# Optimization experiments

Measured on AMD Instinct MI355X. Metric: run time of the kernel, lower is better.

## Reference

```python
import jax, jax.numpy as jnp
import numpy as np

N = 100_000        # number of independent Markov chains (particles)
N_FRAMES = 500     # chain length (module default)
# index 0 -> identity (stay), index 1 -> swap (flip state)
T_MAT = jnp.array([[[1., 0.], [0., 1.]],
                   [[0., 1.], [1., 0.]]], dtype=jnp.float32)


def setup_inputs() -> dict:
    key = jax.random.key(0)
    idx = jax.random.randint(key, (N,), 0, 2)
    initial = jax.nn.one_hot(idx, 2, dtype=jnp.float32)  # one-hot states [N,2]
    return {"initial": initial, "seed": 0}


def reference(initial, seed):
    key = jax.random.key(seed)
    kp, ks = jax.random.split(key)
    # torch code resets transition probs once at i==0 with p = rand()*0.001
    p = jax.random.uniform(kp, (), dtype=jnp.float32) * 0.001
    # row 0: [0.8, 0.2]; row 1: [1-p, p]
    p1 = jnp.stack([jnp.float32(0.2), p])  # P(class==1) per categorical row
    keys = jax.random.split(ks, N_FRAMES)

    def step(state, k):
        # Categorical sample per (particle, row): A[n, j] ~ Bernoulli(p1[j])
        u = jax.random.uniform(k, state.shape, dtype=state.dtype)
        A = (u < p1[None, :]).astype(state.dtype)          # [N,2] in {0,1}
        t = jnp.sum(state * A, axis=-1).astype(jnp.int32)  # [N] select action
        m = T_MAT[t]                                       # [N,2,2] permutation
        new_state = jnp.einsum('nc,ncd->nd', state, m)     # [N,2]
        return new_state, new_state

    _, chain = jax.lax.scan(step, initial, keys)
    return chain  # [N_FRAMES, N, 2]
```

## Files before the change

### kernel.cpp

```cpp
#include <hip/hip_runtime.h>
#include <stdint.h>

#define N_PART   100000
#define N_FRAMES 500

__device__ __forceinline__ uint32_t rotl32(uint32_t v, int d) {
    return (v << d) | (v >> (32 - d));
}

#define TF_ROUND(r) { x0 += x1; x1 = rotl32(x1, (r)); x1 ^= x0; }

__device__ __forceinline__ void tf2x32(uint32_t k0, uint32_t k1,
                                       uint32_t x0, uint32_t x1,
                                       uint32_t &o0, uint32_t &o1) {
    const uint32_t k2 = k0 ^ k1 ^ 0x1BD11BDAu;
    x0 += k0; x1 += k1;
    TF_ROUND(13) TF_ROUND(15) TF_ROUND(26) TF_ROUND(6)
    x0 += k1; x1 += k2 + 1u;
    TF_ROUND(17) TF_ROUND(29) TF_ROUND(16) TF_ROUND(24)
    x0 += k2; x1 += k0 + 2u;
    TF_ROUND(13) TF_ROUND(15) TF_ROUND(26) TF_ROUND(6)
    x0 += k0; x1 += k1 + 3u;
    TF_ROUND(17) TF_ROUND(29) TF_ROUND(16) TF_ROUND(24)
    x0 += k1; x1 += k2 + 4u;
    TF_ROUND(13) TF_ROUND(15) TF_ROUND(26) TF_ROUND(6)
    x0 += k2; x1 += k0 + 5u;
    o0 = x0; o1 = x1;
}

__device__ __forceinline__ float uniform_from_bits(uint32_t bits) {
    return __uint_as_float((bits >> 9) | 0x3f800000u) - 1.0f;
}

__global__ __launch_bounds__(256)
void hmm_kernel(const float* __restrict__ initial,
                const int* __restrict__ seed_ptr,
                float* __restrict__ out) {
    __shared__ uint32_t skey0[N_FRAMES];
    __shared__ uint32_t skey1[N_FRAMES];
    __shared__ float sp;

    const int tid = threadIdx.x;
    const uint32_t seed_lo = (uint32_t)seed_ptr[0];
    const uint32_t seed_hi = 0u;

    uint32_t ks0, ks1;
    tf2x32(seed_hi, seed_lo, 0u, 1u, ks0, ks1);

    for (int t = tid; t < N_FRAMES; t += blockDim.x) {
        uint32_t a, b;
        tf2x32(ks0, ks1, 0u, (uint32_t)t, a, b);
        skey0[t] = a;
        skey1[t] = b;
    }
    if (tid == 0) {
        uint32_t kp0, kp1;
        tf2x32(seed_hi, seed_lo, 0u, 0u, kp0, kp1);
        uint32_t b0, b1;
        tf2x32(kp0, kp1, 0u, 0u, b0, b1);
        sp = uniform_from_bits(b0 ^ b1) * 0.001f;
    }
    __syncthreads();

    const int n = blockIdx.x * blockDim.x + tid;
    if (n >= N_PART) return;

    const float p = sp;
    const float p0 = 0.2f;

    int s = (initial[2 * n + 1] > 0.5f) ? 1 : 0;

    float2* __restrict__ outv = (float2*)out;

    for (int t = 0; t < N_FRAMES; ++t) {
        const uint32_t k0 = skey0[t];
        const uint32_t k1 = skey1[t];
        uint32_t b0, b1;
        tf2x32(k0, k1, 0u, (uint32_t)(2 * n + s), b0, b1);
        const float u = uniform_from_bits(b0 ^ b1);
        const float thr = s ? p : p0;
        s ^= (u < thr) ? 1 : 0;
        const float2 o = s ? make_float2(0.0f, 1.0f) : make_float2(1.0f, 0.0f);
        outv[(size_t)t * N_PART + n] = o;
    }
}

extern "C" void kernel_launch(void* const* d_in, const int* in_sizes, int n_in,
                              void* d_out, int out_size, void* d_ws, size_t ws_size,
                              hipStream_t stream) {
    const float* initial = (const float*)d_in[0];
    const int*   seed    = (const int*)d_in[1];
    float*       out     = (float*)d_out;

    const int block = 256;
    const int grid = (N_PART + block - 1) / block;
    hmm_kernel<<<grid, block, 0, stream>>>(initial, seed, out);
}
```

Before: 497.2 us.

## Split chain simulation into bitmap pass and vectorized streaming output kernel

```diff
diff --git a/kernel.cpp b/kernel.cpp
--- a/kernel.cpp
+++ b/kernel.cpp
@@ -3,6 +3,10 @@
 
 #define N_PART   100000
 #define N_FRAMES 500
+#define NTW      16
+#define PPB      391
+
+typedef float f32x4 __attribute__((ext_vector_type(4)));
 
 __device__ __forceinline__ uint32_t rotl32(uint32_t v, int d) {
     return (v << d) | (v >> (32 - d));
@@ -32,56 +36,75 @@
     return __uint_as_float((bits >> 9) | 0x3f800000u) - 1.0f;
 }
 
-__global__ __launch_bounds__(256)
-void hmm_kernel(const float* __restrict__ initial,
-                const int* __restrict__ seed_ptr,
-                float* __restrict__ out) {
-    __shared__ uint32_t skey0[N_FRAMES];
-    __shared__ uint32_t skey1[N_FRAMES];
-    __shared__ float sp;
+__global__ __launch_bounds__(512)
+void chain_kernel(const float* __restrict__ initial,
+                  const int* __restrict__ seed_ptr,
+                  uint32_t* __restrict__ bmp) {
+    __shared__ uint32_t sk0[N_FRAMES + 1], sk1[N_FRAMES + 1];
+    __shared__ float sp_;
 
     const int tid = threadIdx.x;
     const uint32_t seed_lo = (uint32_t)seed_ptr[0];
-    const uint32_t seed_hi = 0u;
 
-    uint32_t ks0, ks1;
-    tf2x32(seed_hi, seed_lo, 0u, 1u, ks0, ks1);
-
-    for (int t = tid; t < N_FRAMES; t += blockDim.x) {
-        uint32_t a, b;
-        tf2x32(ks0, ks1, 0u, (uint32_t)t, a, b);
-        skey0[t] = a;
-        skey1[t] = b;
+    if (tid <= N_FRAMES) {
+        uint32_t ks0, ks1, a, b;
+        tf2x32(0u, seed_lo, 0u, 1u, ks0, ks1);
+        tf2x32(ks0, ks1, 0u, (uint32_t)tid, a, b);
+        sk0[tid] = a; sk1[tid] = b;
     }
-    if (tid == 0) {
-        uint32_t kp0, kp1;
-        tf2x32(seed_hi, seed_lo, 0u, 0u, kp0, kp1);
-        uint32_t b0, b1;
+    if (tid == 511) {
+        uint32_t kp0, kp1, b0, b1;
+        tf2x32(0u, seed_lo, 0u, 0u, kp0, kp1);
         tf2x32(kp0, kp1, 0u, 0u, b0, b1);
-        sp = uniform_from_bits(b0 ^ b1) * 0.001f;
+        sp_ = uniform_from_bits(b0 ^ b1) * 0.001f;
     }
     __syncthreads();
 
-    const int n = blockIdx.x * blockDim.x + tid;
-    if (n >= N_PART) return;
+    const int n = blockIdx.x * PPB + tid;
+    if (tid >= PPB || n >= N_PART) return;
 
-    const float p = sp;
+    const float p  = sp_;
     const float p0 = 0.2f;
+    const uint32_t base = 2u * (uint32_t)n;
 
-    int s = (initial[2 * n + 1] > 0.5f) ? 1 : 0;
-
-    float2* __restrict__ outv = (float2*)out;
+    uint32_t s = (initial[2 * n + 1] > 0.5f) ? 1u : 0u;
+    uint32_t k0 = sk0[0], k1 = sk1[0];
+    uint32_t bits = 0u;
 
     for (int t = 0; t < N_FRAMES; ++t) {
-        const uint32_t k0 = skey0[t];
-        const uint32_t k1 = skey1[t];
-        uint32_t b0, b1;
-        tf2x32(k0, k1, 0u, (uint32_t)(2 * n + s), b0, b1);
-        const float u = uniform_from_bits(b0 ^ b1);
-        const float thr = s ? p : p0;
-        s ^= (u < thr) ? 1 : 0;
-        const float2 o = s ? make_float2(0.0f, 1.0f) : make_float2(1.0f, 0.0f);
-        outv[(size_t)t * N_PART + n] = o;
+        const uint32_t nk0 = sk0[t + 1], nk1 = sk1[t + 1];
+        uint32_t o0, o1;
+        tf2x32(k0, k1, 0u, base + s, o0, o1);
+        const float u = uniform_from_bits(o0 ^ o1);
+        s ^= (u < (s ? p : p0)) ? 1u : 0u;
+        bits |= s << (t & 31);
+        if ((t & 31) == 31) {
+            bmp[(size_t)(t >> 5) * N_PART + n] = bits;
+            bits = 0u;
+        }
+        k0 = nk0; k1 = nk1;
+    }
+    bmp[(size_t)(NTW - 1) * N_PART + n] = bits;
+}
+
+__global__ __launch_bounds__(256)
+void emit_kernel(const uint32_t* __restrict__ bmp,
+                 f32x4* __restrict__ out4) {
+    const int total = (N_FRAMES * N_PART) / 2;
+    const int stride = gridDim.x * blockDim.x;
+    for (int f = blockIdx.x * blockDim.x + threadIdx.x; f < total; f += stride) {
+        const unsigned t  = (unsigned)f / (N_PART / 2);
+        const unsigned rr = (unsigned)f - t * (N_PART / 2);
+        const unsigned n0 = 2u * rr;
+        const size_t wbase = (size_t)(t >> 5) * N_PART + n0;
+        const uint32_t w0 = bmp[wbase];
+        const uint32_t w1 = bmp[wbase + 1];
+        const uint32_t bit = t & 31u;
+        const float s0 = (float)((w0 >> bit) & 1u);
+        const float s1 = (float)((w1 >> bit) & 1u);
+        f32x4 v;
+        v.x = 1.0f - s0; v.y = s0; v.z = 1.0f - s1; v.w = s1;
+        __builtin_nontemporal_store(v, &out4[f]);
     }
 }
 
@@ -90,9 +113,9 @@
                               hipStream_t stream) {
     const float* initial = (const float*)d_in[0];
     const int*   seed    = (const int*)d_in[1];
-    float*       out     = (float*)d_out;
+    uint32_t*    bmp     = (uint32_t*)d_ws;
+    f32x4*       out4    = (f32x4*)d_out;
 
-    const int block = 256;
-    const int grid = (N_PART + block - 1) / block;
-    hmm_kernel<<<grid, block, 0, stream>>>(initial, seed, out);
+    chain_kernel<<<256, 512, 0, stream>>>(initial, seed, bmp);
+    emit_kernel<<<4096, 256, 0, stream>>>(bmp, out4);
 }
```

Result: slower. 563.0 us (+13.2%).
